# Kernel tuning notes

Hardware: AMD Instinct MI355X
Metric: run time of the kernel (lower is better)

Reference implementation:

```python
import jax, jax.numpy as jnp
import numpy as np

C = 64

def conv2d(x, w, b, pad):
    out = jax.lax.conv_general_dilated(x, w, (1, 1), [(pad, pad), (pad, pad)],
                                       dimension_numbers=('NCHW', 'OIHW', 'NCHW'))
    return out + b[None, :, None, None]


def deform_conv(x, w_off, b_off, w, b, pad):
    # Standard pure-pytorch DeformConv2d (offset conv is 3x3/pad1, sampling on
    # zero-padded input, p0 starts at 1, bilinear gather, then kxk weight contraction).
    ks = w.shape[-1]
    N = ks * ks
    B, Cc, H, W = x.shape
    off = conv2d(x, w_off, b_off, 1)                      # (B, 2N, H, W)
    xp = jnp.pad(x, ((0, 0), (0, 0), (pad, pad), (pad, pad))) if pad > 0 else x
    Hp, Wp = xp.shape[2], xp.shape[3]
    off = off.transpose(0, 2, 3, 1)                       # (B, H, W, 2N)
    r = jnp.arange(-(ks - 1) // 2, (ks - 1) // 2 + 1, dtype=x.dtype)
    pn_x = jnp.repeat(r, ks)                              # (N,) kernel row offsets (n = i*ks + j)
    pn_y = jnp.tile(r, ks)                                # (N,) kernel col offsets
    p0_x = jnp.arange(1, H + 1, dtype=x.dtype)[:, None, None]   # (H,1,1)
    p0_y = jnp.arange(1, W + 1, dtype=x.dtype)[:, None]         # (W,1)
    px = off[..., :N] + p0_x + pn_x                       # (B,H,W,N) sample rows
    py = off[..., N:] + p0_y + pn_y                       # (B,H,W,N) sample cols
    fx = jnp.floor(jax.lax.stop_gradient(px))
    fy = jnp.floor(jax.lax.stop_gradient(py))
    lt_x = jnp.clip(fx, 0, Hp - 1)
    lt_y = jnp.clip(fy, 0, Wp - 1)
    rb_x = jnp.clip(fx + 1, 0, Hp - 1)
    rb_y = jnp.clip(fy + 1, 0, Wp - 1)
    pxc = jnp.clip(px, 0, Hp - 1)
    pyc = jnp.clip(py, 0, Wp - 1)
    g_lt = (1 + (lt_x - pxc)) * (1 + (lt_y - pyc))
    g_rb = (1 - (rb_x - pxc)) * (1 - (rb_y - pyc))
    g_lb = (1 + (lt_x - pxc)) * (1 - (rb_y - pyc))
    g_rt = (1 - (rb_x - pxc)) * (1 + (lt_y - pyc))
    xpf = xp.reshape(B, Cc, Hp * Wp)

    def gather(qx, qy):
        idx = (qx * Wp + qy).astype(jnp.int32).reshape(B, 1, -1)
        g = jnp.take_along_axis(xpf, jnp.broadcast_to(idx, (B, Cc, idx.shape[-1])), axis=2)
        return g.reshape(B, Cc, H, W, N)

    x_off = (g_lt[:, None] * gather(lt_x, lt_y) +
             g_rb[:, None] * gather(rb_x, rb_y) +
             g_lb[:, None] * gather(lt_x, rb_y) +
             g_rt[:, None] * gather(rb_x, lt_y))          # (B,C,H,W,N)
    out = jnp.einsum('bchwn,ocn->bohw', x_off, w.reshape(w.shape[0], Cc, N))
    return out + b[None, :, None, None]


def setup_inputs() -> dict:
    key = jax.random.key(0)
    ks_list = [1, 3, 5]
    keys = jax.random.split(key, 32)
    inp = {'x': jax.random.normal(keys[0], (4, C, 96, 96), dtype=jnp.float32)}
    i = 1
    for ks in ks_list:
        N = ks * ks
        inp[f'wo{ks}'] = jax.random.normal(keys[i], (2 * N, C, 3, 3), dtype=jnp.float32) * 0.01; i += 1
        inp[f'bo{ks}'] = jax.random.normal(keys[i], (2 * N,), dtype=jnp.float32) * 0.01; i += 1
        inp[f'w{ks}'] = jax.random.normal(keys[i], (C, C, ks, ks), dtype=jnp.float32) * 0.05; i += 1
        inp[f'b{ks}'] = jax.random.normal(keys[i], (C,), dtype=jnp.float32) * 0.05; i += 1
        inp[f'wa{ks}'] = jax.random.normal(keys[i], (C, C, ks, ks), dtype=jnp.float32) * 0.05; i += 1
        inp[f'ba{ks}'] = jax.random.normal(keys[i], (C,), dtype=jnp.float32) * 0.05; i += 1
    return inp


def reference(x, wo1, bo1, w1, b1, wa1, ba1, wo3, bo3, w3, b3, wa3, ba3, wo5, bo5, w5, b5, wa5, ba5):
    lrelu = lambda t: jnp.where(t >= 0, t, 0.1 * t)
    x1 = lrelu(deform_conv(x, wo1, bo1, w1, b1, 0))
    x2 = lrelu(deform_conv(x, wo3, bo3, w3, b3, 1))
    x3 = lrelu(deform_conv(x, wo5, bo5, w5, b5, 2))
    msf = x1 + x2 + x3
    att = jax.nn.sigmoid(conv2d(msf, wa1, ba1, 0) + conv2d(msf, wa3, ba3, 1) + conv2d(msf, wa5, ba5, 2))
    return msf * att + msf
```

## Files before the change

### kernel.cpp

```cpp
#include <hip/hip_runtime.h>
#include <math.h>

constexpr int B = 4, C = 64, H = 96, W = 96, HW = H * W;
constexpr int HWP = 100 * 100;

typedef __attribute__((ext_vector_type(8))) short bf16x8;
typedef __attribute__((ext_vector_type(4))) float f32x4;
typedef __attribute__((ext_vector_type(4))) unsigned int uint4v;

constexpr size_t OFF_OFFALL = 0;
constexpr size_t OFF_X1     = OFF_OFFALL + (size_t)B*72*HW;
constexpr size_t OFF_X2     = OFF_X1  + (size_t)B*64*HW;
constexpr size_t OFF_X3     = OFF_X2  + (size_t)B*64*HW;
constexpr size_t OFF_XPAD   = OFF_X3  + (size_t)B*64*HW;
constexpr size_t OFF_MSF    = OFF_XPAD;
constexpr size_t OFF_WOT    = OFF_XPAD + (size_t)B*64*HWP;
constexpr size_t OFF_BOALL  = OFF_WOT + (size_t)64*9*72;
constexpr size_t OFF_WPKH   = OFF_BOALL + 128;
constexpr size_t OFF_WPKL   = OFF_WPKH + 71680;
constexpr size_t OFF_WEFF   = OFF_WPKL + 71680;
constexpr size_t OFF_BEFF   = OFF_WEFF + (size_t)64*25*64;

__global__ void prep_all(const float* __restrict__ wo1, const float* __restrict__ bo1,
                         const float* __restrict__ wo3, const float* __restrict__ bo3,
                         const float* __restrict__ wo5, const float* __restrict__ bo5,
                         const float* __restrict__ w1, const float* __restrict__ w3,
                         const float* __restrict__ w5,
                         const float* __restrict__ wa1, const float* __restrict__ ba1,
                         const float* __restrict__ wa3, const float* __restrict__ ba3,
                         const float* __restrict__ wa5, const float* __restrict__ ba5,
                         float* __restrict__ woT, float* __restrict__ boAll,
                         unsigned short* __restrict__ wPkH, unsigned short* __restrict__ wPkL,
                         float* __restrict__ weff, float* __restrict__ beff) {
  int idx = blockIdx.x * 256 + threadIdx.x;
  if (idx < 41472) {
    int ic = idx / (9 * 72), tap = (idx / 72) % 9, oc = idx % 72;
    float v = 0.f;
    if (oc < 2)       v = wo1[(oc * 64 + ic) * 9 + tap];
    else if (oc < 20) v = wo3[((oc - 2) * 64 + ic) * 9 + tap];
    else if (oc < 70) v = wo5[((oc - 20) * 64 + ic) * 9 + tap];
    woT[idx] = v;
  }
  if (idx < 72) boAll[idx] = idx < 2 ? bo1[idx] : idx < 20 ? bo3[idx - 2] : idx < 70 ? bo5[idx - 20] : 0.f;
  if (idx < 64) beff[idx] = ba1[idx] + ba3[idx] + ba5[idx];
  int i3 = idx - 41472;
  if (i3 >= 0 && i3 < 102400) {
    int ic = i3 / 1600, tap = (i3 / 64) % 25, oc = i3 & 63;
    int kh = tap / 5, kw = tap % 5;
    float v = wa5[(oc * 64 + ic) * 25 + tap];
    if (kh >= 1 && kh <= 3 && kw >= 1 && kw <= 3)
      v += wa3[(oc * 64 + ic) * 9 + (kh - 1) * 3 + (kw - 1)];
    if (tap == 12) v += wa1[oc * 64 + ic];
    weff[i3] = v;
  }
  int e = idx - 143872;
  if (e >= 0 && e < 143360) {
    int i  = e & 7;
    int l  = (e >> 3) & 63;
    int nt = (e >> 9) & 3;
    int kt = (e >> 11) & 1;
    int tap = e >> 12;
    int c  = kt * 32 + 8 * (l >> 4) + i;
    int oc = nt * 16 + (l & 15);
    float w;
    if (tap == 0)      w = w1[oc * 64 + c];
    else if (tap < 10) w = w3[(oc * 64 + c) * 9 + (tap - 1)];
    else               w = w5[(oc * 64 + c) * 25 + (tap - 10)];
    unsigned bits = __float_as_uint(w);
    unsigned hib  = bits & 0xffff0000u;
    float lo = w - __uint_as_float(hib);
    wPkH[e] = (unsigned short)(bits >> 16);
    wPkL[e] = (unsigned short)(__float_as_uint(lo) >> 16);
  }
}

__global__ void pad_x(const float* __restrict__ x, float* __restrict__ xpad) {
  int i = blockIdx.x * 256 + threadIdx.x;
  if (i >= B * 64 * HWP) return;
  int u = i % HWP, bc = i / HWP;
  int r = u / 100, col = u % 100;
  float v = 0.f;
  if (r >= 2 && r < 98 && col >= 2 && col < 98)
    v = x[(size_t)bc * HW + (r - 2) * 96 + (col - 2)];
  xpad[i] = v;
}

__global__ void zero_buf(float* __restrict__ p) {
  int i = blockIdx.x * 256 + threadIdx.x;
  reinterpret_cast<float4*>(p)[i] = make_float4(0.f, 0.f, 0.f, 0.f);
}

template <int NOC, int OCB>
__device__ __forceinline__ void conv_off_body(const float* __restrict__ x,
                                              const float* __restrict__ woT,
                                              const float* __restrict__ boAll,
                                              float* __restrict__ offAll,
                                              float* __restrict__ xs,
                                              float* __restrict__ wsh,
                                              int h, int b, int tid) {
  constexpr int OCPG = NOC / 8;
  const int ocg = tid >> 5, pixg = tid & 31;
  const int oc0 = ocg * OCPG, w0 = pixg * 3;
  float acc[OCPG][3] = {};

  for (int cc = 0; cc < 8; ++cc) {
    __syncthreads();
    for (int idx = tid; idx < 2400; idx += 256) {
      int ic = idx / 300, r = (idx / 100) % 3, j = idx % 100;
      int wc = j - 1, hr = h - 1 + r;
      float v = 0.f;
      if (wc >= 0 && wc < 96 && hr >= 0 && hr < 96)
        v = x[((size_t)(b * 64 + cc * 8 + ic) * 96 + hr) * 96 + wc];
      xs[(ic * 3 + r) * 100 + j] = v;
    }
    for (int i = tid; i < 8 * 9 * NOC; i += 256) {
      int ic = i / (9 * NOC), rem = i % (9 * NOC), tap = rem / NOC, j = rem % NOC;
      wsh[i] = woT[((size_t)(cc * 8 + ic) * 9 + tap) * 72 + OCB + j];
    }
    __syncthreads();
#pragma unroll 2
    for (int ic = 0; ic < 8; ++ic) {
#pragma unroll
      for (int kh = 0; kh < 3; ++kh) {
        float xv[5];
#pragma unroll
        for (int t = 0; t < 5; ++t) xv[t] = xs[(ic * 3 + kh) * 100 + w0 + t];
#pragma unroll
        for (int kw = 0; kw < 3; ++kw) {
          const float* wrow = &wsh[(ic * 9 + kh * 3 + kw) * NOC + oc0];
#pragma unroll
          for (int o = 0; o < OCPG; ++o) {
            float wv = wrow[o];
            acc[o][0] += wv * xv[kw + 0];
            acc[o][1] += wv * xv[kw + 1];
            acc[o][2] += wv * xv[kw + 2];
          }
        }
      }
    }
  }
#pragma unroll
  for (int o = 0; o < OCPG; ++o) {
    int oc = OCB + oc0 + o;
    float bias = boAll[oc];
#pragma unroll
    for (int p = 0; p < 3; ++p)
      offAll[((size_t)(b * 72 + oc) * 96 + h) * 96 + w0 + p] = acc[o][p] + bias;
  }
}

__global__ __launch_bounds__(256) void conv_off(const float* __restrict__ x,
                                                const float* __restrict__ woT,
                                                const float* __restrict__ boAll,
                                                float* __restrict__ offAll) {
  __shared__ __align__(16) float xs[8 * 3 * 100];
  __shared__ __align__(16) float wsh[8 * 9 * 40];
  const int h = blockIdx.x, b = blockIdx.y, tid = threadIdx.x;
  if (blockIdx.z == 0) conv_off_body<40, 0>(x, woT, boAll, offAll, xs, wsh, h, b, tid);
  else                 conv_off_body<32, 40>(x, woT, boAll, offAll, xs, wsh, h, b, tid);
}

template <int KS, bool ATOMIC>
__device__ __forceinline__ void deform_mfma_body(const float* __restrict__ xpb,
                                                 const float* __restrict__ offAll,
                                                 const unsigned short* __restrict__ wPkH,
                                                 const unsigned short* __restrict__ wPkL,
                                                 float* __restrict__ dst,
                                                 int n0, int n1, int b, int h0,
                                                 int* __restrict__ spb, int* __restrict__ spd,
                                                 float* __restrict__ spg, int tid) {
  constexpr int N = KS * KS, P = (KS - 1) / 2, S = 2 - P, HP = H + 2 * P;
  constexpr int CHB = KS == 1 ? 0 : KS == 3 ? 2 : 20;
  constexpr int GB  = KS == 1 ? 0 : KS == 3 ? 1 : 10;
  const int lane = tid & 63, wv = tid >> 6;
  const int pxw = wv * 48, lg = lane >> 4, lm = lane & 15;
  f32x4 acc[3][4];
#pragma unroll
  for (int a1 = 0; a1 < 3; ++a1)
#pragma unroll
    for (int a2 = 0; a2 < 4; ++a2) acc[a1][a2] = (f32x4)0.f;

  for (int n = n0; n < n1; ++n) {
    if (tid < 192) {
      int w = tid % 96, r = tid / 96, h = h0 + r;
      float ox = offAll[((size_t)(b * 72 + CHB + n) * 96 + h) * 96 + w];
      float oy = offAll[((size_t)(b * 72 + CHB + N + n) * 96 + h) * 96 + w];
      float px = ox + (float)(h + 1 + n / KS - P);
      float py = oy + (float)(w + 1 + n % KS - P);
      float fx = floorf(px), fy = floorf(py);
      float hpm = (float)(HP - 1);
      float ltx = fminf(fmaxf(fx, 0.f), hpm);
      float rbx = fminf(fmaxf(fx + 1.f, 0.f), hpm);
      float lty = fminf(fmaxf(fy, 0.f), hpm);
      float rby = fminf(fmaxf(fy + 1.f, 0.f), hpm);
      float pxc = fminf(fmaxf(px, 0.f), hpm);
      float pyc = fminf(fmaxf(py, 0.f), hpm);
      float gx0 = 1.f + (ltx - pxc);
      float gx1 = 1.f - (rbx - pxc);
      float gy0 = 1.f + (lty - pyc);
      float gy1 = 1.f - (rby - pyc);
      int ix0 = (int)ltx, ix1 = (int)rbx, iy0 = (int)lty, iy1 = (int)rby;
      spb[tid] = (ix0 + S) * 100 + iy0 + S;
      spd[tid] = (ix1 - ix0) * 100 + ((iy1 - iy0) << 16);
      spg[0 * 192 + tid] = gx0 * gy0;
      spg[1 * 192 + tid] = gx1 * gy1;
      spg[2 * 192 + tid] = gx0 * gy1;
      spg[3 * 192 + tid] = gx1 * gy0;
    }
    __syncthreads();
#pragma unroll
    for (int kt = 0; kt < 2; ++kt) {
      const int bb = (((GB + n) * 2 + kt)) * 256 + lane;
      uint4v bh[4], bl[4];
#pragma unroll
      for (int nt = 0; nt < 4; ++nt) {
        bh[nt] = reinterpret_cast<const uint4v*>(wPkH)[bb + nt * 64];
        bl[nt] = reinterpret_cast<const uint4v*>(wPkL)[bb + nt * 64];
      }
#pragma unroll
      for (int mt = 0; mt < 3; ++mt) {
        int px = pxw + mt * 16 + lm;
        int base = spb[px];
        int d = spd[px];
        int dx = d & 0xffff, dy = d >> 16;
        float g0 = spg[px], g1 = spg[192 + px], g2 = spg[384 + px], g3 = spg[576 + px];
        const float* xc = xpb + (kt * 32 + lg * 8) * HWP + base;
        float vv[8];
#pragma unroll
        for (int i = 0; i < 8; ++i) {
          const float* p = xc + i * HWP;
          vv[i] = g0 * p[0] + g1 * p[dx + dy] + g2 * p[dy] + g3 * p[dx];
        }
        unsigned hp[4], lp[4];
#pragma unroll
        for (int j = 0; j < 4; ++j) {
          unsigned b0 = __float_as_uint(vv[2 * j]), b1 = __float_as_uint(vv[2 * j + 1]);
          unsigned h0b = b0 & 0xffff0000u, h1b = b1 & 0xffff0000u;
          float l0 = vv[2 * j] - __uint_as_float(h0b);
          float l1 = vv[2 * j + 1] - __uint_as_float(h1b);
          hp[j] = (b0 >> 16) | h1b;
          lp[j] = (__float_as_uint(l0) >> 16) | (__float_as_uint(l1) & 0xffff0000u);
        }
        uint4v hv = {hp[0], hp[1], hp[2], hp[3]};
        uint4v lv = {lp[0], lp[1], lp[2], lp[3]};
        bf16x8 ah = __builtin_bit_cast(bf16x8, hv);
        bf16x8 al = __builtin_bit_cast(bf16x8, lv);
#pragma unroll
        for (int nt = 0; nt < 4; ++nt) {
          bf16x8 BH = __builtin_bit_cast(bf16x8, bh[nt]);
          bf16x8 BL = __builtin_bit_cast(bf16x8, bl[nt]);
          acc[mt][nt] = __builtin_amdgcn_mfma_f32_16x16x32_bf16(ah, BH, acc[mt][nt], 0, 0, 0);
          acc[mt][nt] = __builtin_amdgcn_mfma_f32_16x16x32_bf16(al, BH, acc[mt][nt], 0, 0, 0);
          acc[mt][nt] = __builtin_amdgcn_mfma_f32_16x16x32_bf16(ah, BL, acc[mt][nt], 0, 0, 0);
        }
      }
    }
    __syncthreads();
  }
#pragma unroll
  for (int mt = 0; mt < 3; ++mt) {
#pragma unroll
    for (int reg = 0; reg < 4; ++reg) {
      int px = pxw + mt * 16 + lg * 4 + reg;
      int rr = px >= 96 ? 1 : 0;
      int wcol = px - rr * 96;
#pragma unroll
      for (int nt = 0; nt < 4; ++nt) {
        int oc = nt * 16 + lm;
        size_t ai = ((size_t)(b * 64 + oc) * 96 + h0 + rr) * 96 + wcol;
        float val = acc[mt][nt][reg];
        if (ATOMIC) atomicAdd(&dst[ai], val);
        else        dst[ai] = val;
      }
    }
  }
}

__global__ __launch_bounds__(256, 3) void deform_mfma(const float* __restrict__ xpad,
                                                      const float* __restrict__ offAll,
                                                      const unsigned short* __restrict__ wPkH,
                                                      const unsigned short* __restrict__ wPkL,
                                                      float* __restrict__ x1,
                                                      float* __restrict__ x2,
                                                      float* __restrict__ x3) {
  __shared__ int spb[192], spd[192];
  __shared__ float spg[4 * 192];
  int bid = blockIdx.x;
  int typ = bid & 3, idx = bid >> 2;
  int h0 = (idx % 48) * 2, b = idx / 48;
  int tid = threadIdx.x;
  const float* xpb = xpad + (size_t)b * 64 * HWP;
  if (typ == 0)
    deform_mfma_body<5, true>(xpb, offAll, wPkH, wPkL, x3, 0, 9, b, h0, spb, spd, spg, tid);
  else if (typ == 1)
    deform_mfma_body<5, true>(xpb, offAll, wPkH, wPkL, x3, 9, 17, b, h0, spb, spd, spg, tid);
  else if (typ == 2)
    deform_mfma_body<5, true>(xpb, offAll, wPkH, wPkL, x3, 17, 25, b, h0, spb, spd, spg, tid);
  else {
    deform_mfma_body<3, false>(xpb, offAll, wPkH, wPkL, x2, 0, 9, b, h0, spb, spd, spg, tid);
    deform_mfma_body<1, false>(xpb, offAll, wPkH, wPkL, x1, 0, 1, b, h0, spb, spd, spg, tid);
  }
}

__global__ __launch_bounds__(256) void msf_build(const float* __restrict__ x1,
                                                 const float* __restrict__ x2,
                                                 const float* __restrict__ x3,
                                                 const float* __restrict__ b1,
                                                 const float* __restrict__ b3,
                                                 const float* __restrict__ b5,
                                                 float* __restrict__ msf) {
  int i = blockIdx.x * 256 + threadIdx.x;
  int c = (i / 2304) & 63;
  float bb1 = b1[c], bb3 = b3[c], bb5 = b5[c];
  float4 v1 = reinterpret_cast<const float4*>(x1)[i];
  float4 v2 = reinterpret_cast<const float4*>(x2)[i];
  float4 v3 = reinterpret_cast<const float4*>(x3)[i];
  float4 m;
  float a1, a2, a3;
  a1 = v1.x + bb1; a1 = a1 >= 0.f ? a1 : 0.1f * a1;
  a2 = v2.x + bb3; a2 = a2 >= 0.f ? a2 : 0.1f * a2;
  a3 = v3.x + bb5; a3 = a3 >= 0.f ? a3 : 0.1f * a3;
  m.x = a1 + a2 + a3;
  a1 = v1.y + bb1; a1 = a1 >= 0.f ? a1 : 0.1f * a1;
  a2 = v2.y + bb3; a2 = a2 >= 0.f ? a2 : 0.1f * a2;
  a3 = v3.y + bb5; a3 = a3 >= 0.f ? a3 : 0.1f * a3;
  m.y = a1 + a2 + a3;
  a1 = v1.z + bb1; a1 = a1 >= 0.f ? a1 : 0.1f * a1;
  a2 = v2.z + bb3; a2 = a2 >= 0.f ? a2 : 0.1f * a2;
  a3 = v3.z + bb5; a3 = a3 >= 0.f ? a3 : 0.1f * a3;
  m.z = a1 + a2 + a3;
  a1 = v1.w + bb1; a1 = a1 >= 0.f ? a1 : 0.1f * a1;
  a2 = v2.w + bb3; a2 = a2 >= 0.f ? a2 : 0.1f * a2;
  a3 = v3.w + bb5; a3 = a3 >= 0.f ? a3 : 0.1f * a3;
  m.w = a1 + a2 + a3;
  reinterpret_cast<float4*>(msf)[i] = m;
}

__global__ __launch_bounds__(128) void att_final(const float* __restrict__ msf,
                                                 const float* __restrict__ weff,
                                                 const float* __restrict__ beff,
                                                 float* __restrict__ out) {
  __shared__ __align__(16) float xs[4 * 5 * 100];
  __shared__ __align__(16) float wsh[4 * 25 * 16];
  const int h = blockIdx.x, b = blockIdx.y, zoc = blockIdx.z * 16;
  const int tid = threadIdx.x;
  const int ocg = tid >> 5, colg = tid & 31;
  const int oc0 = ocg * 4, w0 = colg * 3;
  float acc[4][3] = {};

  for (int cc = 0; cc < 16; ++cc) {
    __syncthreads();
    for (int idx = tid; idx < 2000; idx += 128) {
      int ic = idx / 500, r = (idx / 100) % 5, j = idx % 100;
      int hr = h - 2 + r, wc = j - 2;
      float v = 0.f;
      if (hr >= 0 && hr < 96 && wc >= 0 && wc < 96)
        v = msf[((size_t)(b * 64 + cc * 4 + ic) * 96 + hr) * 96 + wc];
      xs[idx] = v;
    }
    for (int i = tid; i < 400; i += 128) {
      int ict = i >> 2, q = i & 3;
      int ic = ict / 25, tap = ict % 25;
      reinterpret_cast<float4*>(wsh)[i] =
          *reinterpret_cast<const float4*>(weff + ((size_t)(cc * 4 + ic) * 25 + tap) * 64 + zoc + q * 4);
    }
    __syncthreads();
#pragma unroll
    for (int ic = 0; ic < 4; ++ic) {
#pragma unroll
      for (int kh = 0; kh < 5; ++kh) {
        float xv[7];
#pragma unroll
        for (int t = 0; t < 7; ++t) xv[t] = xs[ic * 500 + kh * 100 + w0 + t];
#pragma unroll
        for (int kw = 0; kw < 5; ++kw) {
          const float4 wv = *reinterpret_cast<const float4*>(&wsh[(ic * 25 + kh * 5 + kw) * 16 + oc0]);
          float wvv[4] = {wv.x, wv.y, wv.z, wv.w};
#pragma unroll
          for (int o = 0; o < 4; ++o) {
            acc[o][0] += wvv[o] * xv[kw + 0];
            acc[o][1] += wvv[o] * xv[kw + 1];
            acc[o][2] += wvv[o] * xv[kw + 2];
          }
        }
      }
    }
  }
#pragma unroll
  for (int o = 0; o < 4; ++o) {
    int oc = zoc + oc0 + o;
    float bz = beff[oc];
#pragma unroll
    for (int p = 0; p < 3; ++p) {
      float z = acc[o][p] + bz;
      float att = 1.f / (1.f + __expf(-z));
      size_t oi = ((size_t)(b * 64 + oc) * 96 + h) * 96 + w0 + p;
      float m = msf[oi];
      out[oi] = m + m * att;
    }
  }
}

extern "C" void kernel_launch(void* const* d_in, const int* in_sizes, int n_in,
                              void* d_out, int out_size, void* d_ws, size_t ws_size,
                              hipStream_t stream) {
  const float* x   = (const float*)d_in[0];
  const float* wo1 = (const float*)d_in[1];
  const float* bo1 = (const float*)d_in[2];
  const float* w1  = (const float*)d_in[3];
  const float* b1  = (const float*)d_in[4];
  const float* wa1 = (const float*)d_in[5];
  const float* ba1 = (const float*)d_in[6];
  const float* wo3 = (const float*)d_in[7];
  const float* bo3 = (const float*)d_in[8];
  const float* w3  = (const float*)d_in[9];
  const float* b3  = (const float*)d_in[10];
  const float* wa3 = (const float*)d_in[11];
  const float* ba3 = (const float*)d_in[12];
  const float* wo5 = (const float*)d_in[13];
  const float* bo5 = (const float*)d_in[14];
  const float* w5  = (const float*)d_in[15];
  const float* b5  = (const float*)d_in[16];
  const float* wa5 = (const float*)d_in[17];
  const float* ba5 = (const float*)d_in[18];

  float* ws     = (float*)d_ws;
  float* offAll = ws + OFF_OFFALL;
  float* x1     = ws + OFF_X1;
  float* x2     = ws + OFF_X2;
  float* x3     = ws + OFF_X3;
  float* xpad   = ws + OFF_XPAD;
  float* msf    = ws + OFF_MSF;
  float* woT    = ws + OFF_WOT;
  float* boAll  = ws + OFF_BOALL;
  unsigned short* wPkH = (unsigned short*)(ws + OFF_WPKH);
  unsigned short* wPkL = (unsigned short*)(ws + OFF_WPKL);
  float* weff   = ws + OFF_WEFF;
  float* beff   = ws + OFF_BEFF;

  float* out = (float*)d_out;

  hipLaunchKernelGGL(prep_all, dim3(1122), dim3(256), 0, stream,
                     wo1, bo1, wo3, bo3, wo5, bo5, w1, w3, w5,
                     wa1, ba1, wa3, ba3, wa5, ba5,
                     woT, boAll, wPkH, wPkL, weff, beff);
  hipLaunchKernelGGL(pad_x, dim3(10000), dim3(256), 0, stream, x, xpad);
  hipLaunchKernelGGL(zero_buf, dim3(2304), dim3(256), 0, stream, x3);
  hipLaunchKernelGGL(conv_off, dim3(96, 4, 2), dim3(256), 0, stream, x, woT, boAll, offAll);
  hipLaunchKernelGGL(deform_mfma, dim3(768), dim3(256), 0, stream,
                     xpad, offAll, wPkH, wPkL, x1, x2, x3);
  hipLaunchKernelGGL(msf_build, dim3(2304), dim3(256), 0, stream,
                     x1, x2, x3, b1, b3, b5, msf);
  hipLaunchKernelGGL(att_final, dim3(96, 4, 4), dim3(128), 0, stream,
                     msf, weff, beff, out);
}
```

Measured before the change: 705.5 us.

## Drop padded input and atomics, double-buffer sample tables, remap blocks

Removes the pad_x and zero_buf kernels. Deformable sampling now reads the unpadded input directly, with clamped indices and validity masks folded into the bilinear weights. The 5x5 branch writes three partial buffers that msf_build sums, replacing atomicAdd into a zeroed buffer. Sampling tables in shared memory are double-buffered so one barrier per tap can be dropped, and all kernels use a 1D grid that interleaves batch and row halves. att_final also moves to 256 threads with 32 output channels per block, and msf now aliases the offset buffer.

```diff
diff --git a/kernel.cpp b/kernel.cpp
--- a/kernel.cpp
+++ b/kernel.cpp
@@ -2,19 +2,19 @@
 #include <math.h>
 
 constexpr int B = 4, C = 64, H = 96, W = 96, HW = H * W;
-constexpr int HWP = 100 * 100;
 
 typedef __attribute__((ext_vector_type(8))) short bf16x8;
 typedef __attribute__((ext_vector_type(4))) float f32x4;
 typedef __attribute__((ext_vector_type(4))) unsigned int uint4v;
 
 constexpr size_t OFF_OFFALL = 0;
+constexpr size_t OFF_MSF    = OFF_OFFALL;
 constexpr size_t OFF_X1     = OFF_OFFALL + (size_t)B*72*HW;
 constexpr size_t OFF_X2     = OFF_X1  + (size_t)B*64*HW;
-constexpr size_t OFF_X3     = OFF_X2  + (size_t)B*64*HW;
-constexpr size_t OFF_XPAD   = OFF_X3  + (size_t)B*64*HW;
-constexpr size_t OFF_MSF    = OFF_XPAD;
-constexpr size_t OFF_WOT    = OFF_XPAD + (size_t)B*64*HWP;
+constexpr size_t OFF_X3A    = OFF_X2  + (size_t)B*64*HW;
+constexpr size_t OFF_X3B    = OFF_X3A + (size_t)B*64*HW;
+constexpr size_t OFF_X3C    = OFF_X3B + (size_t)B*64*HW;
+constexpr size_t OFF_WOT    = OFF_X3C + (size_t)B*64*HW;
 constexpr size_t OFF_BOALL  = OFF_WOT + (size_t)64*9*72;
 constexpr size_t OFF_WPKH   = OFF_BOALL + 128;
 constexpr size_t OFF_WPKL   = OFF_WPKH + 71680;
@@ -74,22 +74,6 @@
   }
 }
 
-__global__ void pad_x(const float* __restrict__ x, float* __restrict__ xpad) {
-  int i = blockIdx.x * 256 + threadIdx.x;
-  if (i >= B * 64 * HWP) return;
-  int u = i % HWP, bc = i / HWP;
-  int r = u / 100, col = u % 100;
-  float v = 0.f;
-  if (r >= 2 && r < 98 && col >= 2 && col < 98)
-    v = x[(size_t)bc * HW + (r - 2) * 96 + (col - 2)];
-  xpad[i] = v;
-}
-
-__global__ void zero_buf(float* __restrict__ p) {
-  int i = blockIdx.x * 256 + threadIdx.x;
-  reinterpret_cast<float4*>(p)[i] = make_float4(0.f, 0.f, 0.f, 0.f);
-}
-
 template <int NOC, int OCB>
 __device__ __forceinline__ void conv_off_body(const float* __restrict__ x,
                                               const float* __restrict__ woT,
@@ -155,13 +139,16 @@
                                                 float* __restrict__ offAll) {
   __shared__ __align__(16) float xs[8 * 3 * 100];
   __shared__ __align__(16) float wsh[8 * 9 * 40];
-  const int h = blockIdx.x, b = blockIdx.y, tid = threadIdx.x;
-  if (blockIdx.z == 0) conv_off_body<40, 0>(x, woT, boAll, offAll, xs, wsh, h, b, tid);
-  else                 conv_off_body<32, 40>(x, woT, boAll, offAll, xs, wsh, h, b, tid);
-}
-
-template <int KS, bool ATOMIC>
-__device__ __forceinline__ void deform_mfma_body(const float* __restrict__ xpb,
+  const int bid = blockIdx.x, tid = threadIdx.x;
+  const int r = bid & 7, q = bid >> 3;
+  const int b = r >> 1, half = r & 1;
+  const int z = q & 1, h = half * 48 + (q >> 1);
+  if (z == 0) conv_off_body<40, 0>(x, woT, boAll, offAll, xs, wsh, h, b, tid);
+  else        conv_off_body<32, 40>(x, woT, boAll, offAll, xs, wsh, h, b, tid);
+}
+
+template <int KS>
+__device__ __forceinline__ void deform_mfma_body(const float* __restrict__ xb,
                                                  const float* __restrict__ offAll,
                                                  const unsigned short* __restrict__ wPkH,
                                                  const unsigned short* __restrict__ wPkL,
@@ -169,7 +156,7 @@
                                                  int n0, int n1, int b, int h0,
                                                  int* __restrict__ spb, int* __restrict__ spd,
                                                  float* __restrict__ spg, int tid) {
-  constexpr int N = KS * KS, P = (KS - 1) / 2, S = 2 - P, HP = H + 2 * P;
+  constexpr int N = KS * KS, P = (KS - 1) / 2, HP = H + 2 * P;
   constexpr int CHB = KS == 1 ? 0 : KS == 3 ? 2 : 20;
   constexpr int GB  = KS == 1 ? 0 : KS == 3 ? 1 : 10;
   const int lane = tid & 63, wv = tid >> 6;
@@ -181,31 +168,42 @@
     for (int a2 = 0; a2 < 4; ++a2) acc[a1][a2] = (f32x4)0.f;
 
   for (int n = n0; n < n1; ++n) {
+    const int buf = n & 1;
+    int* sb = spb + buf * 192;
+    int* sd = spd + buf * 192;
+    float* sg = spg + buf * 768;
     if (tid < 192) {
-      int w = tid % 96, r = tid / 96, h = h0 + r;
+      int w = tid % 96, rr = tid / 96, h = h0 + rr;
       float ox = offAll[((size_t)(b * 72 + CHB + n) * 96 + h) * 96 + w];
       float oy = offAll[((size_t)(b * 72 + CHB + N + n) * 96 + h) * 96 + w];
-      float px = ox + (float)(h + 1 + n / KS - P);
-      float py = oy + (float)(w + 1 + n % KS - P);
-      float fx = floorf(px), fy = floorf(py);
+      float pxf = ox + (float)(h + 1 + n / KS - P);
+      float pyf = oy + (float)(w + 1 + n % KS - P);
+      float fx = floorf(pxf), fy = floorf(pyf);
       float hpm = (float)(HP - 1);
       float ltx = fminf(fmaxf(fx, 0.f), hpm);
       float rbx = fminf(fmaxf(fx + 1.f, 0.f), hpm);
       float lty = fminf(fmaxf(fy, 0.f), hpm);
       float rby = fminf(fmaxf(fy + 1.f, 0.f), hpm);
-      float pxc = fminf(fmaxf(px, 0.f), hpm);
-      float pyc = fminf(fmaxf(py, 0.f), hpm);
+      float pxc = fminf(fmaxf(pxf, 0.f), hpm);
+      float pyc = fminf(fmaxf(pyf, 0.f), hpm);
       float gx0 = 1.f + (ltx - pxc);
       float gx1 = 1.f - (rbx - pxc);
       float gy0 = 1.f + (lty - pyc);
       float gy1 = 1.f - (rby - pyc);
-      int ix0 = (int)ltx, ix1 = (int)rbx, iy0 = (int)lty, iy1 = (int)rby;
-      spb[tid] = (ix0 + S) * 100 + iy0 + S;
-      spd[tid] = (ix1 - ix0) * 100 + ((iy1 - iy0) << 16);
-      spg[0 * 192 + tid] = gx0 * gy0;
-      spg[1 * 192 + tid] = gx1 * gy1;
-      spg[2 * 192 + tid] = gx0 * gy1;
-      spg[3 * 192 + tid] = gx1 * gy0;
+      int rx0 = (int)ltx - P, rx1 = (int)rbx - P;
+      int ry0 = (int)lty - P, ry1 = (int)rby - P;
+      float vx0 = (rx0 >= 0 && rx0 < 96) ? 1.f : 0.f;
+      float vx1 = (rx1 >= 0 && rx1 < 96) ? 1.f : 0.f;
+      float vy0 = (ry0 >= 0 && ry0 < 96) ? 1.f : 0.f;
+      float vy1 = (ry1 >= 0 && ry1 < 96) ? 1.f : 0.f;
+      int cx0 = min(max(rx0, 0), 95), cx1 = min(max(rx1, 0), 95);
+      int cy0 = min(max(ry0, 0), 95), cy1 = min(max(ry1, 0), 95);
+      sb[tid] = cx0 * 96 + cy0;
+      sd[tid] = (cx1 - cx0) * 96 | ((cy1 - cy0) << 16);
+      sg[0 * 192 + tid] = gx0 * gy0 * vx0 * vy0;
+      sg[1 * 192 + tid] = gx1 * gy1 * vx1 * vy1;
+      sg[2 * 192 + tid] = gx0 * gy1 * vx0 * vy1;
+      sg[3 * 192 + tid] = gx1 * gy0 * vx1 * vy0;
     }
     __syncthreads();
 #pragma unroll
@@ -220,15 +218,15 @@
 #pragma unroll
       for (int mt = 0; mt < 3; ++mt) {
         int px = pxw + mt * 16 + lm;
-        int base = spb[px];
-        int d = spd[px];
+        int base = sb[px];
+        int d = sd[px];
         int dx = d & 0xffff, dy = d >> 16;
-        float g0 = spg[px], g1 = spg[192 + px], g2 = spg[384 + px], g3 = spg[576 + px];
-        const float* xc = xpb + (kt * 32 + lg * 8) * HWP + base;
+        float g0 = sg[px], g1 = sg[192 + px], g2 = sg[384 + px], g3 = sg[576 + px];
+        const float* xc = xb + (size_t)(kt * 32 + lg * 8) * HW + base;
         float vv[8];
 #pragma unroll
         for (int i = 0; i < 8; ++i) {
-          const float* p = xc + i * HWP;
+          const float* p = xc + (size_t)i * HW;
           vv[i] = g0 * p[0] + g1 * p[dx + dy] + g2 * p[dy] + g3 * p[dx];
         }
         unsigned hp[4], lp[4];
@@ -255,7 +253,6 @@
         }
       }
     }
-    __syncthreads();
   }
 #pragma unroll
   for (int mt = 0; mt < 3; ++mt) {
@@ -267,44 +264,47 @@
 #pragma unroll
       for (int nt = 0; nt < 4; ++nt) {
         int oc = nt * 16 + lm;
-        size_t ai = ((size_t)(b * 64 + oc) * 96 + h0 + rr) * 96 + wcol;
-        float val = acc[mt][nt][reg];
-        if (ATOMIC) atomicAdd(&dst[ai], val);
-        else        dst[ai] = val;
+        dst[((size_t)(b * 64 + oc) * 96 + h0 + rr) * 96 + wcol] = acc[mt][nt][reg];
       }
     }
   }
 }
 
-__global__ __launch_bounds__(256, 3) void deform_mfma(const float* __restrict__ xpad,
+__global__ __launch_bounds__(256, 3) void deform_mfma(const float* __restrict__ x,
                                                       const float* __restrict__ offAll,
                                                       const unsigned short* __restrict__ wPkH,
                                                       const unsigned short* __restrict__ wPkL,
                                                       float* __restrict__ x1,
                                                       float* __restrict__ x2,
-                                                      float* __restrict__ x3) {
-  __shared__ int spb[192], spd[192];
-  __shared__ float spg[4 * 192];
-  int bid = blockIdx.x;
-  int typ = bid & 3, idx = bid >> 2;
-  int h0 = (idx % 48) * 2, b = idx / 48;
-  int tid = threadIdx.x;
-  const float* xpb = xpad + (size_t)b * 64 * HWP;
+                                                      float* __restrict__ x3a,
+                                                      float* __restrict__ x3b,
+                                                      float* __restrict__ x3c) {
+  __shared__ int spb[2 * 192], spd[2 * 192];
+  __shared__ float spg[2 * 768];
+  const int bid = blockIdx.x, tid = threadIdx.x;
+  const int r = bid & 7, q = bid >> 3;
+  const int b = r >> 1, half = r & 1;
+  const int typ = q & 3, strip = half * 24 + (q >> 2);
+  const int h0 = strip * 2;
+  const float* xb = x + (size_t)b * 64 * HW;
   if (typ == 0)
-    deform_mfma_body<5, true>(xpb, offAll, wPkH, wPkL, x3, 0, 9, b, h0, spb, spd, spg, tid);
+    deform_mfma_body<5>(xb, offAll, wPkH, wPkL, x3a, 0, 9, b, h0, spb, spd, spg, tid);
   else if (typ == 1)
-    deform_mfma_body<5, true>(xpb, offAll, wPkH, wPkL, x3, 9, 17, b, h0, spb, spd, spg, tid);
+    deform_mfma_body<5>(xb, offAll, wPkH, wPkL, x3b, 9, 17, b, h0, spb, spd, spg, tid);
   else if (typ == 2)
-    deform_mfma_body<5, true>(xpb, offAll, wPkH, wPkL, x3, 17, 25, b, h0, spb, spd, spg, tid);
+    deform_mfma_body<5>(xb, offAll, wPkH, wPkL, x3c, 17, 25, b, h0, spb, spd, spg, tid);
   else {
-    deform_mfma_body<3, false>(xpb, offAll, wPkH, wPkL, x2, 0, 9, b, h0, spb, spd, spg, tid);
-    deform_mfma_body<1, false>(xpb, offAll, wPkH, wPkL, x1, 0, 1, b, h0, spb, spd, spg, tid);
+    deform_mfma_body<3>(xb, offAll, wPkH, wPkL, x2, 0, 9, b, h0, spb, spd, spg, tid);
+    __syncthreads();
+    deform_mfma_body<1>(xb, offAll, wPkH, wPkL, x1, 0, 1, b, h0, spb, spd, spg, tid);
   }
 }
 
 __global__ __launch_bounds__(256) void msf_build(const float* __restrict__ x1,
                                                  const float* __restrict__ x2,
-                                                 const float* __restrict__ x3,
+                                                 const float* __restrict__ x3a,
+                                                 const float* __restrict__ x3b,
+                                                 const float* __restrict__ x3c,
                                                  const float* __restrict__ b1,
                                                  const float* __restrict__ b3,
                                                  const float* __restrict__ b5,
@@ -314,55 +314,60 @@
   float bb1 = b1[c], bb3 = b3[c], bb5 = b5[c];
   float4 v1 = reinterpret_cast<const float4*>(x1)[i];
   float4 v2 = reinterpret_cast<const float4*>(x2)[i];
-  float4 v3 = reinterpret_cast<const float4*>(x3)[i];
+  float4 va = reinterpret_cast<const float4*>(x3a)[i];
+  float4 vb = reinterpret_cast<const float4*>(x3b)[i];
+  float4 vc = reinterpret_cast<const float4*>(x3c)[i];
   float4 m;
   float a1, a2, a3;
   a1 = v1.x + bb1; a1 = a1 >= 0.f ? a1 : 0.1f * a1;
   a2 = v2.x + bb3; a2 = a2 >= 0.f ? a2 : 0.1f * a2;
-  a3 = v3.x + bb5; a3 = a3 >= 0.f ? a3 : 0.1f * a3;
+  a3 = va.x + vb.x + vc.x + bb5; a3 = a3 >= 0.f ? a3 : 0.1f * a3;
   m.x = a1 + a2 + a3;
   a1 = v1.y + bb1; a1 = a1 >= 0.f ? a1 : 0.1f * a1;
   a2 = v2.y + bb3; a2 = a2 >= 0.f ? a2 : 0.1f * a2;
-  a3 = v3.y + bb5; a3 = a3 >= 0.f ? a3 : 0.1f * a3;
+  a3 = va.y + vb.y + vc.y + bb5; a3 = a3 >= 0.f ? a3 : 0.1f * a3;
   m.y = a1 + a2 + a3;
   a1 = v1.z + bb1; a1 = a1 >= 0.f ? a1 : 0.1f * a1;
   a2 = v2.z + bb3; a2 = a2 >= 0.f ? a2 : 0.1f * a2;
-  a3 = v3.z + bb5; a3 = a3 >= 0.f ? a3 : 0.1f * a3;
+  a3 = va.z + vb.z + vc.z + bb5; a3 = a3 >= 0.f ? a3 : 0.1f * a3;
   m.z = a1 + a2 + a3;
   a1 = v1.w + bb1; a1 = a1 >= 0.f ? a1 : 0.1f * a1;
   a2 = v2.w + bb3; a2 = a2 >= 0.f ? a2 : 0.1f * a2;
-  a3 = v3.w + bb5; a3 = a3 >= 0.f ? a3 : 0.1f * a3;
+  a3 = va.w + vb.w + vc.w + bb5; a3 = a3 >= 0.f ? a3 : 0.1f * a3;
   m.w = a1 + a2 + a3;
   reinterpret_cast<float4*>(msf)[i] = m;
 }
 
-__global__ __launch_bounds__(128) void att_final(const float* __restrict__ msf,
+__global__ __launch_bounds__(256) void att_final(const float* __restrict__ msf,
                                                  const float* __restrict__ weff,
                                                  const float* __restrict__ beff,
                                                  float* __restrict__ out) {
   __shared__ __align__(16) float xs[4 * 5 * 100];
-  __shared__ __align__(16) float wsh[4 * 25 * 16];
-  const int h = blockIdx.x, b = blockIdx.y, zoc = blockIdx.z * 16;
-  const int tid = threadIdx.x;
+  __shared__ __align__(16) float wsh[4 * 25 * 32];
+  const int bid = blockIdx.x, tid = threadIdx.x;
+  const int r = bid & 7, q = bid >> 3;
+  const int b = r >> 1, half = r & 1;
+  const int zhalf = q & 1, h = half * 48 + (q >> 1);
+  const int zoc = zhalf * 32;
   const int ocg = tid >> 5, colg = tid & 31;
   const int oc0 = ocg * 4, w0 = colg * 3;
   float acc[4][3] = {};
 
   for (int cc = 0; cc < 16; ++cc) {
     __syncthreads();
-    for (int idx = tid; idx < 2000; idx += 128) {
-      int ic = idx / 500, r = (idx / 100) % 5, j = idx % 100;
-      int hr = h - 2 + r, wc = j - 2;
+    for (int idx = tid; idx < 2000; idx += 256) {
+      int ic = idx / 500, rr = (idx / 100) % 5, j = idx % 100;
+      int hr = h - 2 + rr, wc = j - 2;
       float v = 0.f;
       if (hr >= 0 && hr < 96 && wc >= 0 && wc < 96)
         v = msf[((size_t)(b * 64 + cc * 4 + ic) * 96 + hr) * 96 + wc];
       xs[idx] = v;
     }
-    for (int i = tid; i < 400; i += 128) {
-      int ict = i >> 2, q = i & 3;
+    for (int i = tid; i < 800; i += 256) {
+      int ict = i >> 3, qq = i & 7;
       int ic = ict / 25, tap = ict % 25;
       reinterpret_cast<float4*>(wsh)[i] =
-          *reinterpret_cast<const float4*>(weff + ((size_t)(cc * 4 + ic) * 25 + tap) * 64 + zoc + q * 4);
+          *reinterpret_cast<const float4*>(weff + ((size_t)(cc * 4 + ic) * 25 + tap) * 64 + zoc + qq * 4);
     }
     __syncthreads();
 #pragma unroll
@@ -374,7 +379,7 @@
         for (int t = 0; t < 7; ++t) xv[t] = xs[ic * 500 + kh * 100 + w0 + t];
 #pragma unroll
         for (int kw = 0; kw < 5; ++kw) {
-          const float4 wv = *reinterpret_cast<const float4*>(&wsh[(ic * 25 + kh * 5 + kw) * 16 + oc0]);
+          const float4 wv = *reinterpret_cast<const float4*>(&wsh[(ic * 25 + kh * 5 + kw) * 32 + oc0]);
           float wvv[4] = {wv.x, wv.y, wv.z, wv.w};
 #pragma unroll
           for (int o = 0; o < 4; ++o) {
@@ -426,11 +431,12 @@
 
   float* ws     = (float*)d_ws;
   float* offAll = ws + OFF_OFFALL;
+  float* msf    = ws + OFF_MSF;
   float* x1     = ws + OFF_X1;
   float* x2     = ws + OFF_X2;
-  float* x3     = ws + OFF_X3;
-  float* xpad   = ws + OFF_XPAD;
-  float* msf    = ws + OFF_MSF;
+  float* x3a    = ws + OFF_X3A;
+  float* x3b    = ws + OFF_X3B;
+  float* x3c    = ws + OFF_X3C;
   float* woT    = ws + OFF_WOT;
   float* boAll  = ws + OFF_BOALL;
   unsigned short* wPkH = (unsigned short*)(ws + OFF_WPKH);
@@ -444,13 +450,11 @@
                      wo1, bo1, wo3, bo3, wo5, bo5, w1, w3, w5,
                      wa1, ba1, wa3, ba3, wa5, ba5,
                      woT, boAll, wPkH, wPkL, weff, beff);
-  hipLaunchKernelGGL(pad_x, dim3(10000), dim3(256), 0, stream, x, xpad);
-  hipLaunchKernelGGL(zero_buf, dim3(2304), dim3(256), 0, stream, x3);
-  hipLaunchKernelGGL(conv_off, dim3(96, 4, 2), dim3(256), 0, stream, x, woT, boAll, offAll);
+  hipLaunchKernelGGL(conv_off, dim3(768), dim3(256), 0, stream, x, woT, boAll, offAll);
   hipLaunchKernelGGL(deform_mfma, dim3(768), dim3(256), 0, stream,
-                     xpad, offAll, wPkH, wPkL, x1, x2, x3);
+                     x, offAll, wPkH, wPkL, x1, x2, x3a, x3b, x3c);
   hipLaunchKernelGGL(msf_build, dim3(2304), dim3(256), 0, stream,
-                     x1, x2, x3, b1, b3, b5, msf);
-  hipLaunchKernelGGL(att_final, dim3(96, 4, 4), dim3(128), 0, stream,
+                     x1, x2, x3a, x3b, x3c, b1, b3, b5, msf);
+  hipLaunchKernelGGL(att_final, dim3(768), dim3(256), 0, stream,
                      msf, weff, beff, out);
 }
```

Measured after the change: 609.8 us. 13.6% less time.
